# Kernel tuning notes

Hardware: AMD Instinct MI355X
Metric: run time of the kernel (lower is better)

The kernel has to match this reference:

```python
import jax, jax.numpy as jnp
from jax import lax
import numpy as np

VOCAB = 2048
EMB = 256
LAT = 128
MAX_SENLEN = 8
SIZE_LAT = 3.0
BATCH = 32


def lm_softmax(tokens, E, Wi, Wh, b):
    """Embedding(mask_zero) -> LSTM(units=VOCAB) -> softmax. tokens: [B, L] int."""
    B, L = tokens.shape
    emb = E[tokens]                      # [B, L, EMB]
    mask = (tokens != 0)                 # PAD==0 is masked (Keras mask_zero)
    H = Wh.shape[0]

    def step(carry, xm):
        h, c = carry
        x, m = xm                        # x: [B, EMB], m: [B]
        gates = x @ Wi + h @ Wh + b      # [B, 4H], Keras gate order i,f,g,o
        i, f, g, o = jnp.split(gates, 4, axis=1)
        i = jax.nn.sigmoid(i)
        f = jax.nn.sigmoid(f)
        g = jnp.tanh(g)
        o = jax.nn.sigmoid(o)
        c_new = f * c + i * g
        h_new = o * jnp.tanh(c_new)
        m = m[:, None]
        h = jnp.where(m, h_new, h)       # masked steps carry state through
        c = jnp.where(m, c_new, c)
        return (h, c), None

    h0 = jnp.zeros((B, H), emb.dtype)
    (h, _), _ = lax.scan(step, (h0, h0), (jnp.swapaxes(emb, 0, 1), mask.T))
    return jax.nn.softmax(h, axis=-1)    # [B, VOCAB]


def setup_inputs() -> dict:
    key = jax.random.key(0)
    k1, k2, k3, k4 = jax.random.split(key, 4)
    input_tokens = jax.random.randint(k1, (BATCH, MAX_SENLEN), 0, VOCAB, dtype=jnp.int32)
    E = jax.random.normal(k2, (VOCAB, EMB), jnp.float32) * 0.02
    Wi = jax.random.normal(k3, (EMB, 4 * VOCAB), jnp.float32) * 0.02
    Wh = jax.random.normal(k4, (VOCAB, 4 * VOCAB), jnp.float32) * 0.02
    b = jnp.zeros((4 * VOCAB,), jnp.float32).at[VOCAB:2 * VOCAB].set(1.0)  # unit_forget_bias
    return {"input_tokens": input_tokens, "E": E, "Wi": Wi, "Wh": Wh, "b": b}


def reference(input_tokens, E, Wi, Wh, b):
    """Unrolled DAriEL_Encoder_Cell_2 RNN: returns z sequence [B, T, LAT]."""
    B, T = input_tokens.shape
    tokens = jnp.zeros((B, T + 1), jnp.int32)        # tokens state, col 0 = PAD
    # RNN zero initial state: bounds both zero at t=0 (cond keeps them since timeStep==0)
    low = jnp.zeros((B, LAT), jnp.float32)
    upp = jnp.zeros((B, LAT), jnp.float32)
    outs = []
    for t in range(T):
        # replace_column(tokens, input_token, timeStep+1)
        tokens = tokens.at[:, t + 1].set(input_tokens[:, t])
        if t > 0:  # tf.cond(mean(timeStep) > 0, initial bounds, state bounds)
            low = jnp.zeros((B, LAT), jnp.float32)
            upp = jnp.full((B, LAT), SIZE_LAT, jnp.float32)
        sm = lm_softmax(tokens[:, : t + 1], E, Wi, Wh, b)   # LM on prefix s_0toj
        s_j = tokens[:, t + 1]                               # current token
        c_inc = jnp.cumsum(sm, axis=1)
        c_exc = c_inc - sm
        cu = jnp.take_along_axis(c_inc, s_j[:, None], axis=1)  # [B,1]
        cl = jnp.take_along_axis(c_exc, s_j[:, None], axis=1)  # [B,1]
        rng = upp - low
        new_low = low + rng * cl
        upp = low + rng * cu
        low = new_low
        z = (low + upp) * 0.5            # mean over stacked bounds
        outs.append(z)
    return jnp.stack(outs, axis=1)       # [B, T, LAT]
```

## Files before the change

### kernel.cpp

```cpp
#include <hip/hip_runtime.h>

#define BATCH 32
#define TT 8
#define VOCAB 2048
#define EMB 256
#define NG 8192
#define LAT 128
#define KTOT 2304
#define NKT 72
#define NJT 128

#define WSCALE 4096.0f
#define ASCALE 16.0f
#define DQ (1.0f/65536.0f)

typedef float f32x4 __attribute__((ext_vector_type(4)));

#define EAC_OFF 0
#define FLG_OFF 256
#define EPC_OFF 4352
#define ZP_OFF  4368
#define SP_OFF  33040
#define AFX_OFF 61712
#define AFH_OFF 76048
#define BP_OFF  108816

#define AT_LD(p)    __hip_atomic_load((p),  __ATOMIC_RELAXED, __HIP_MEMORY_SCOPE_AGENT)
#define AT_ST(p,v)  __hip_atomic_store((p), (v), __ATOMIC_RELAXED, __HIP_MEMORY_SCOPE_AGENT)

__device__ __forceinline__ float sigmoidf_(float x){ return 1.f/(1.f+__expf(-x)); }
__device__ __forceinline__ float tanhf_(float x){
  x = fminf(fmaxf(x, -10.f), 10.f);
  float e = __expf(2.f*x);
  return (e-1.f)/(e+1.f);
}
__device__ __forceinline__ unsigned char f2e4m3(float f){
  const unsigned int u = __float_as_uint(f);
  const unsigned int sign = (u >> 24) & 0x80u;
  const unsigned int au = u & 0x7FFFFFFFu;
  const unsigned int r = au + 0x0007FFFFu + ((au >> 20) & 1u);
  unsigned int code = (((r >> 23) - 120u) << 3) | ((r >> 20) & 7u);
  code = (code > 0x7Eu) ? 0x7Eu : code;
  const float a = __uint_as_float(au);
  const unsigned int sub = (unsigned int)rintf(a * 512.0f);
  code = (au < 0x3C800000u) ? sub : code;
  return (unsigned char)(sign | code);
}

__global__ __launch_bounds__(256) void k_pack(
    const int* __restrict__ tok, const float* __restrict__ E,
    const float* __restrict__ Wi, const float* __restrict__ Wh,
    unsigned long long* __restrict__ Bp,
    unsigned long long* __restrict__ AfX, unsigned long long* __restrict__ AfH1,
    int* __restrict__ flg, float* __restrict__ out){
  const int tid = threadIdx.x;
  const int nb = blockIdx.x;
  const int kt = blockIdx.y;
  __shared__ unsigned char lds[32][64];
  {
    const int kl = tid >> 3;
    const int n0 = (tid & 7) * 8;
    const int k  = kt*32 + kl;
    const float* W = (k < EMB) ? (Wi + (size_t)k*NG) : (Wh + (size_t)(k-EMB)*NG);
    const float4 f0 = *(const float4*)(W + nb*64 + n0);
    const float4 f1 = *(const float4*)(W + nb*64 + n0 + 4);
    unsigned long long pk = 0ull;
    pk |= (unsigned long long)f2e4m3(f0.x*WSCALE);
    pk |= (unsigned long long)f2e4m3(f0.y*WSCALE) << 8;
    pk |= (unsigned long long)f2e4m3(f0.z*WSCALE) << 16;
    pk |= (unsigned long long)f2e4m3(f0.w*WSCALE) << 24;
    pk |= (unsigned long long)f2e4m3(f1.x*WSCALE) << 32;
    pk |= (unsigned long long)f2e4m3(f1.y*WSCALE) << 40;
    pk |= (unsigned long long)f2e4m3(f1.z*WSCALE) << 48;
    pk |= (unsigned long long)f2e4m3(f1.w*WSCALE) << 56;
    *(unsigned long long*)&lds[kl][n0] = pk;
  }
  __syncthreads();
  {
    const int ntl = tid >> 6, lane = tid & 63;
    const int kgrp = lane >> 4, n16 = lane & 15;
    unsigned long long pk = 0ull;
    #pragma unroll
    for (int p=0;p<8;p++)
      pk |= ((unsigned long long)lds[kgrp*8 + p][ntl*16 + n16]) << (8*p);
    Bp[((size_t)(nb*4 + ntl)*NKT + kt)*64 + lane] = pk;
  }
  const int i = (kt*128 + nb)*256 + tid;
  if (i < 7*32*32){
    const int s   = i >> 10;
    const int rem = i & 1023;
    const int b   = rem >> 5;
    const int kgi = rem & 31;
    const int tk  = tok[b*TT + s];
    const float4 e0 = *(const float4*)(E + (size_t)tk*EMB + kgi*8);
    const float4 e1 = *(const float4*)(E + (size_t)tk*EMB + kgi*8 + 4);
    unsigned long long pk = 0ull;
    pk |= (unsigned long long)f2e4m3(e0.x*ASCALE);
    pk |= (unsigned long long)f2e4m3(e0.y*ASCALE) << 8;
    pk |= (unsigned long long)f2e4m3(e0.z*ASCALE) << 16;
    pk |= (unsigned long long)f2e4m3(e0.w*ASCALE) << 24;
    pk |= (unsigned long long)f2e4m3(e1.x*ASCALE) << 32;
    pk |= (unsigned long long)f2e4m3(e1.y*ASCALE) << 40;
    pk |= (unsigned long long)f2e4m3(e1.z*ASCALE) << 48;
    pk |= (unsigned long long)f2e4m3(e1.w*ASCALE) << 56;
    AfX[((size_t)((s*2 + (b>>4))*8 + (kgi>>2)))*64 + (kgi&3)*16 + (b&15)] = pk;
  }
  if (i < 8192) AfH1[i] = 0ull;
  if (i < BATCH*LAT)
    out[(size_t)((i>>7)*TT + 0)*LAT + (i&(LAT-1))] = 0.f;
  if (i < 4112) flg[i] = 0;
}

__global__ __launch_bounds__(256, 1) void k_fused(
    const int* __restrict__ tok, const float* __restrict__ bias,
    float* __restrict__ out, float* __restrict__ Zp, float* __restrict__ Sp,
    float* __restrict__ Eac, const unsigned long long* __restrict__ AfX,
    unsigned long long* __restrict__ AfH, const unsigned long long* __restrict__ Bp,
    int* __restrict__ flg){
  const int tid = threadIdx.x;
  const int bid = blockIdx.x;
  const int jt = bid & 127, mh = bid >> 7;
  const int g = tid >> 6, lane = tid & 63;
  const int quad = lane >> 4, col = lane & 15;
  int* __restrict__ epc = flg + 4096;

  __shared__ float gsh[4][16][16];
  __shared__ long hlds[64][64];
  __shared__ unsigned char hsh[256];
  __shared__ float zsh[2];

  const long* __restrict__ BpV = (const long*)Bp;
  const size_t bbase = (size_t)(g*NJT + jt)*NKT*64 + lane;
  long Breg[NKT];
  #pragma unroll
  for (int i=0;i<NKT;i++) Breg[i] = BpV[bbase + (size_t)i*64];
  #pragma unroll
  for (int i=0;i<NKT;i++) asm volatile("" : "+v"(Breg[i]));

  const int b16 = tid >> 4, jj = tid & 15;
  const int b = mh*16 + b16;
  const int j = jt*16 + jj;
  const float bi  = bias[j];
  const float bff = bias[j + VOCAB];
  const float bgg = bias[j + 2*VOCAB];
  const float boo = bias[j + 3*VOCAB];
  const int hoff = ((jj>>3)&1)*128 + b16*8 + (jj&7);
  const size_t bofs = (size_t)(mh*64 + (jt>>1))*512 + (size_t)(jt&1)*256;
  float hreg = 0.f, creg = 0.f;

  for (int t=1; t<TT; t++){
    const long* __restrict__ aX = (const long*)AfX + (size_t)((t-1)*2 + mh)*512 + lane;
    f32x4 acc = {0,0,0,0};
    #pragma unroll
    for (int kt=0; kt<8; kt++)
      acc = __builtin_amdgcn_mfma_f32_16x16x32_fp8_fp8(aX[(size_t)kt*64], Breg[kt], acc, 0,0,0);

    if (t >= 2){
      const int want = t-1;
      if (bid == 255){
        if (tid < 64){
          for (;;){
            int done = 1;
            #pragma unroll
            for (int q2=0;q2<4;q2++)
              done &= (AT_LD(&flg[(tid*4+q2)*16]) >= want) ? 1 : 0;
            if (done) break;
            __builtin_amdgcn_s_sleep(1);
          }
        }
        __syncthreads();
        if (tid == 0) AT_ST(epc, want);
      } else {
        if (tid == 0){
          while (AT_LD(epc) < want) __builtin_amdgcn_s_sleep(1);
        }
      }
      asm volatile("" ::: "memory");
    }
    __syncthreads();

    {
      unsigned long long* aH = AfH + (size_t)(t&1)*8192 + (size_t)mh*4096;
      long hl[16];
      #pragma unroll
      for (int i=0;i<16;i++)
        hl[i] = (long)AT_LD(&aH[(size_t)(g*16+i)*64 + lane]);
      #pragma unroll
      for (int i=0;i<16;i++) hlds[g*16+i][lane] = hl[i];
    }
    __syncthreads();

    #pragma unroll
    for (int kt=8; kt<NKT; kt++)
      acc = __builtin_amdgcn_mfma_f32_16x16x32_fp8_fp8(hlds[kt-8][lane], Breg[kt], acc, 0,0,0);
    #pragma unroll
    for (int r=0;r<4;r++) gsh[g][quad*4 + r][col] = acc[r];
    __syncthreads();

    const float ip = gsh[0][b16][jj]*DQ + bi;
    const float fp = gsh[1][b16][jj]*DQ + bff;
    const float gg = gsh[2][b16][jj]*DQ + bgg;
    const float op = gsh[3][b16][jj]*DQ + boo;
    const float cn = sigmoidf_(fp)*creg + sigmoidf_(ip)*tanhf_(gg);
    const float hn = sigmoidf_(op)*tanhf_(cn);
    if (tok[b*TT + (t-1)] != 0){ hreg = hn; creg = cn; }
    hsh[hoff] = f2e4m3(ASCALE*hreg);
    const int sj = tok[b*TT + t];
    const float e = __expf(hreg);
    if (j == sj) AT_ST(&Eac[(t-1)*32 + b], e);
    float z = e, s = (j < sj) ? e : 0.f;
    #pragma unroll
    for (int m=1; m<16; m<<=1){ z += __shfl_xor(z, m); s += __shfl_xor(s, m); }
    if (jj == 0){
      AT_ST(&Zp[((size_t)(t-1)*32 + b)*128 + jt], z);
      AT_ST(&Sp[((size_t)(t-1)*32 + b)*128 + jt], s);
    }
    __syncthreads();

    if (tid < 32){
      unsigned long long* dst =
        (unsigned long long*)((unsigned char*)AfH + (size_t)((t&1)^1)*65536 + bofs);
      AT_ST(&dst[tid], ((const unsigned long long*)hsh)[tid]);
    }
    asm volatile("s_waitcnt vmcnt(0)" ::: "memory");
    __syncthreads();
    if (tid == 0) AT_ST(&flg[bid*16], t);

    if (t >= 2 && bid < BATCH){
      const int s = t-2;
      if (tid < 64){
        float zl = AT_LD(&Zp[((size_t)s*32+bid)*128 + tid])
                 + AT_LD(&Zp[((size_t)s*32+bid)*128 + tid + 64]);
        float sl = AT_LD(&Sp[((size_t)s*32+bid)*128 + tid])
                 + AT_LD(&Sp[((size_t)s*32+bid)*128 + tid + 64]);
        #pragma unroll
        for (int m=1; m<64; m<<=1){ zl += __shfl_xor(zl, m); sl += __shfl_xor(sl, m); }
        if (tid == 0){ zsh[0] = zl; zsh[1] = sl; }
      }
      __syncthreads();
      if (tid < LAT){
        const float Ej = AT_LD(&Eac[s*32 + bid]);
        out[((size_t)bid*TT + (t-1))*LAT + tid] = (3.f*zsh[1] + 1.5f*Ej)/zsh[0];
      }
    }
  }

  if (bid == 255){
    if (tid < 64){
      for (;;){
        int done = 1;
        #pragma unroll
        for (int q2=0;q2<4;q2++)
          done &= (AT_LD(&flg[(tid*4+q2)*16]) >= TT-1) ? 1 : 0;
        if (done) break;
        __builtin_amdgcn_s_sleep(1);
      }
    }
    __syncthreads();
    if (tid == 0) AT_ST(epc, TT-1);
  }
  if (bid < BATCH){
    if (tid == 0){
      while (AT_LD(epc) < TT-1) __builtin_amdgcn_s_sleep(1);
    }
    asm volatile("" ::: "memory");
    __syncthreads();
    const int s = TT-2;
    if (tid < 64){
      float zl = AT_LD(&Zp[((size_t)s*32+bid)*128 + tid])
               + AT_LD(&Zp[((size_t)s*32+bid)*128 + tid + 64]);
      float sl = AT_LD(&Sp[((size_t)s*32+bid)*128 + tid])
               + AT_LD(&Sp[((size_t)s*32+bid)*128 + tid + 64]);
      #pragma unroll
      for (int m=1; m<64; m<<=1){ zl += __shfl_xor(zl, m); sl += __shfl_xor(sl, m); }
      if (tid == 0){ zsh[0] = zl; zsh[1] = sl; }
    }
    __syncthreads();
    if (tid < LAT){
      const float Ej = AT_LD(&Eac[s*32 + bid]);
      out[((size_t)bid*TT + (TT-1))*LAT + tid] = (3.f*zsh[1] + 1.5f*Ej)/zsh[0];
    }
  }
}

extern "C" void kernel_launch(void* const* d_in, const int* in_sizes, int n_in,
                              void* d_out, int out_size, void* d_ws, size_t ws_size,
                              hipStream_t stream){
  const int*   tok  = (const int*)d_in[0];
  const float* E    = (const float*)d_in[1];
  const float* Wi   = (const float*)d_in[2];
  const float* Wh   = (const float*)d_in[3];
  const float* bias = (const float*)d_in[4];
  float* out = (float*)d_out;
  float* ws  = (float*)d_ws;
  float* Eac = ws + EAC_OFF;
  int*   flg = (int*)(ws + FLG_OFF);
  float* Zp  = ws + ZP_OFF;
  float* Sp  = ws + SP_OFF;
  unsigned long long* AfX = (unsigned long long*)(ws + AFX_OFF);
  unsigned long long* AfH = (unsigned long long*)(ws + AFH_OFF);
  unsigned long long* Bp  = (unsigned long long*)(ws + BP_OFF);

  k_pack<<<dim3(128, NKT), 256, 0, stream>>>(tok, E, Wi, Wh, Bp, AfX, AfH + 8192,
                                             flg, out);
  k_fused<<<256, 256, 0, stream>>>(tok, bias, out, Zp, Sp, Eac, AfX, AfH, Bp, flg);
}
```

Measured before the change: 142.9 us.

## Merge batch halves into 512-thread blocks and use decentralized grid barrier

Halves the grid from 256 to 128 blocks by giving each block both batch halves (8 waves), so each block handles one j-tile for all 32 rows. The two-level barrier through a coordinator block and epoch counter is replaced: every block polls the 128 per-block flags directly. Token values are preloaded into registers. The aim is fewer blocks to synchronize and one fewer hop of global-memory latency per step. The cost is more polling traffic from every block, and with 72 long registers per lane the 512-thread blocks raise register pressure under the new launch bounds.

```diff
diff --git a/kernel.cpp b/kernel.cpp
--- a/kernel.cpp
+++ b/kernel.cpp
@@ -18,7 +18,6 @@
 
 #define EAC_OFF 0
 #define FLG_OFF 256
-#define EPC_OFF 4352
 #define ZP_OFF  4368
 #define SP_OFF  33040
 #define AFX_OFF 61712
@@ -108,10 +107,10 @@
   if (i < 8192) AfH1[i] = 0ull;
   if (i < BATCH*LAT)
     out[(size_t)((i>>7)*TT + 0)*LAT + (i&(LAT-1))] = 0.f;
-  if (i < 4112) flg[i] = 0;
-}
-
-__global__ __launch_bounds__(256, 1) void k_fused(
+  if (i < 4096) flg[i] = 0;
+}
+
+__global__ __launch_bounds__(512, 2) void k_fused(
     const int* __restrict__ tok, const float* __restrict__ bias,
     float* __restrict__ out, float* __restrict__ Zp, float* __restrict__ Sp,
     float* __restrict__ Eac, const unsigned long long* __restrict__ AfX,
@@ -119,14 +118,14 @@
     int* __restrict__ flg){
   const int tid = threadIdx.x;
   const int bid = blockIdx.x;
-  const int jt = bid & 127, mh = bid >> 7;
-  const int g = tid >> 6, lane = tid & 63;
+  const int jt = bid;
+  const int wid = tid >> 6, lane = tid & 63;
+  const int g = wid & 3, mh = wid >> 2;
   const int quad = lane >> 4, col = lane & 15;
-  int* __restrict__ epc = flg + 4096;
-
-  __shared__ float gsh[4][16][16];
-  __shared__ long hlds[64][64];
-  __shared__ unsigned char hsh[256];
+
+  __shared__ float gsh[2][4][16][16];
+  __shared__ long hlds[2][64][64];
+  __shared__ unsigned char hsh[512];
   __shared__ float zsh[2];
 
   const long* __restrict__ BpV = (const long*)Bp;
@@ -137,15 +136,17 @@
   #pragma unroll
   for (int i=0;i<NKT;i++) asm volatile("" : "+v"(Breg[i]));
 
-  const int b16 = tid >> 4, jj = tid & 15;
-  const int b = mh*16 + b16;
+  const int b = tid >> 4, jj = tid & 15;
+  const int b16 = b & 15, mhb = b >> 4;
   const int j = jt*16 + jj;
   const float bi  = bias[j];
   const float bff = bias[j + VOCAB];
   const float bgg = bias[j + 2*VOCAB];
   const float boo = bias[j + 3*VOCAB];
-  const int hoff = ((jj>>3)&1)*128 + b16*8 + (jj&7);
-  const size_t bofs = (size_t)(mh*64 + (jt>>1))*512 + (size_t)(jt&1)*256;
+  int tokr[TT];
+  #pragma unroll
+  for (int q2=0;q2<TT;q2++) tokr[q2] = tok[b*TT + q2];
+  const int hoff = mhb*256 + ((jj>>3)&1)*128 + b16*8 + (jj&7);
   float hreg = 0.f, creg = 0.f;
 
   for (int t=1; t<TT; t++){
@@ -157,22 +158,14 @@
 
     if (t >= 2){
       const int want = t-1;
-      if (bid == 255){
-        if (tid < 64){
-          for (;;){
-            int done = 1;
-            #pragma unroll
-            for (int q2=0;q2<4;q2++)
-              done &= (AT_LD(&flg[(tid*4+q2)*16]) >= want) ? 1 : 0;
-            if (done) break;
-            __builtin_amdgcn_s_sleep(1);
-          }
-        }
-        __syncthreads();
-        if (tid == 0) AT_ST(epc, want);
-      } else {
-        if (tid == 0){
-          while (AT_LD(epc) < want) __builtin_amdgcn_s_sleep(1);
+      if (tid < 64){
+        for (;;){
+          int done = 1;
+          #pragma unroll
+          for (int q2=0;q2<2;q2++)
+            done &= (AT_LD(&flg[(tid*2+q2)*16]) >= want) ? 1 : 0;
+          if (done) break;
+          __builtin_amdgcn_s_sleep(1);
         }
       }
       asm volatile("" ::: "memory");
@@ -186,26 +179,26 @@
       for (int i=0;i<16;i++)
         hl[i] = (long)AT_LD(&aH[(size_t)(g*16+i)*64 + lane]);
       #pragma unroll
-      for (int i=0;i<16;i++) hlds[g*16+i][lane] = hl[i];
+      for (int i=0;i<16;i++) hlds[mh][g*16+i][lane] = hl[i];
     }
     __syncthreads();
 
     #pragma unroll
     for (int kt=8; kt<NKT; kt++)
-      acc = __builtin_amdgcn_mfma_f32_16x16x32_fp8_fp8(hlds[kt-8][lane], Breg[kt], acc, 0,0,0);
-    #pragma unroll
-    for (int r=0;r<4;r++) gsh[g][quad*4 + r][col] = acc[r];
-    __syncthreads();
-
-    const float ip = gsh[0][b16][jj]*DQ + bi;
-    const float fp = gsh[1][b16][jj]*DQ + bff;
-    const float gg = gsh[2][b16][jj]*DQ + bgg;
-    const float op = gsh[3][b16][jj]*DQ + boo;
+      acc = __builtin_amdgcn_mfma_f32_16x16x32_fp8_fp8(hlds[mh][kt-8][lane], Breg[kt], acc, 0,0,0);
+    #pragma unroll
+    for (int r=0;r<4;r++) gsh[mh][g][quad*4 + r][col] = acc[r];
+    __syncthreads();
+
+    const float ip = gsh[mhb][0][b16][jj]*DQ + bi;
+    const float fp = gsh[mhb][1][b16][jj]*DQ + bff;
+    const float gg = gsh[mhb][2][b16][jj]*DQ + bgg;
+    const float op = gsh[mhb][3][b16][jj]*DQ + boo;
     const float cn = sigmoidf_(fp)*creg + sigmoidf_(ip)*tanhf_(gg);
     const float hn = sigmoidf_(op)*tanhf_(cn);
-    if (tok[b*TT + (t-1)] != 0){ hreg = hn; creg = cn; }
+    if (tokr[t-1] != 0){ hreg = hn; creg = cn; }
     hsh[hoff] = f2e4m3(ASCALE*hreg);
-    const int sj = tok[b*TT + t];
+    const int sj = tokr[t];
     const float e = __expf(hreg);
     if (j == sj) AT_ST(&Eac[(t-1)*32 + b], e);
     float z = e, s = (j < sj) ? e : 0.f;
@@ -217,10 +210,12 @@
     }
     __syncthreads();
 
-    if (tid < 32){
+    if (tid < 64){
+      const int pm = tid >> 5, w = tid & 31;
       unsigned long long* dst =
-        (unsigned long long*)((unsigned char*)AfH + (size_t)((t&1)^1)*65536 + bofs);
-      AT_ST(&dst[tid], ((const unsigned long long*)hsh)[tid]);
+        (unsigned long long*)((unsigned char*)AfH + (size_t)((t&1)^1)*65536
+                              + (size_t)(pm*64 + (jt>>1))*512 + (size_t)(jt&1)*256);
+      AT_ST(&dst[w], ((const unsigned long long*)hsh)[pm*32 + w]);
     }
     asm volatile("s_waitcnt vmcnt(0)" ::: "memory");
     __syncthreads();
@@ -245,23 +240,16 @@
     }
   }
 
-  if (bid == 255){
+  if (bid < BATCH){
     if (tid < 64){
       for (;;){
         int done = 1;
         #pragma unroll
-        for (int q2=0;q2<4;q2++)
-          done &= (AT_LD(&flg[(tid*4+q2)*16]) >= TT-1) ? 1 : 0;
+        for (int q2=0;q2<2;q2++)
+          done &= (AT_LD(&flg[(tid*2+q2)*16]) >= TT-1) ? 1 : 0;
         if (done) break;
         __builtin_amdgcn_s_sleep(1);
       }
-    }
-    __syncthreads();
-    if (tid == 0) AT_ST(epc, TT-1);
-  }
-  if (bid < BATCH){
-    if (tid == 0){
-      while (AT_LD(epc) < TT-1) __builtin_amdgcn_s_sleep(1);
     }
     asm volatile("" ::: "memory");
     __syncthreads();
@@ -303,5 +291,5 @@
 
   k_pack<<<dim3(128, NKT), 256, 0, stream>>>(tok, E, Wi, Wh, Bp, AfX, AfH + 8192,
                                              flg, out);
-  k_fused<<<256, 256, 0, stream>>>(tok, bias, out, Zp, Sp, Eac, AfX, AfH, Bp, flg);
-}
+  k_fused<<<128, 512, 0, stream>>>(tok, bias, out, Zp, Sp, Eac, AfX, AfH, Bp, flg);
+}
```

New measurement: 148.3 us. +3.8%, slower.
